# Kernel optimization log

Hardware: AMD Instinct MI355X
Metric: run time of the kernel (lower is better)

The kernel has to match this reference:

```python
import jax, jax.numpy as jnp
import numpy as np

E = 2048        # embed_dim
H = 16          # num_heads
D = 128         # head_dim
K = 4           # num_hyper_nodes (timelines)
N = 4096        # seq_len
B = 1           # batch (module asserts batch==1)
CAP_FACTOR = 1.25
CAP = int(N / K * CAP_FACTOR)   # 1280, static
ROPE_BASE = 10000.0
SCALE = D ** -0.5
NEG_INF = jnp.float32(-1e30)


def setup_inputs() -> dict:
    key = jax.random.key(0)
    ks = jax.random.split(key, 10)
    def xavier(k, shape):
        fan_in, fan_out = shape[0], shape[1]
        lim = np.sqrt(6.0 / (fan_in + fan_out))
        return jax.random.uniform(k, shape, jnp.float32, -lim, lim)
    return {
        'x':   jax.random.normal(ks[0], (B, N, E), jnp.float32),
        # weights stored (in, out); equivalent to torch Linear weight.T
        'Wq':  xavier(ks[1], (E, H * D)),
        'Wk':  xavier(ks[2], (E, H * D)),
        'Wv':  xavier(ks[3], (E, H * D)),
        'Wo':  xavier(ks[4], (H * D, E)),
        'Wr1': xavier(ks[5], (E, E // 2)),
        'br1': jnp.zeros((E // 2,), jnp.float32),
        'Wr2': xavier(ks[6], (E // 2, K)),
        'br2': jnp.zeros((K,), jnp.float32),
    }


def _rope_tables():
    # local positions: arange(CAP) (use_local_rope=True)
    inv_freq = 1.0 / (ROPE_BASE ** (jnp.arange(0, D, 2, dtype=jnp.float32) / D))
    freqs = jnp.arange(CAP, dtype=jnp.float32)[:, None] * inv_freq[None, :]  # (CAP, D/2)
    emb = jnp.concatenate([freqs, freqs], axis=-1)  # (CAP, D)
    return jnp.cos(emb), jnp.sin(emb)


def _rotate_half(t):
    return jnp.concatenate([-t[..., D // 2:], t[..., :D // 2]], axis=-1)


def reference(x, Wq, Wk, Wv, Wo, Wr1, br1, Wr2, br2):
    # --- expert-choice routing ---
    h = jax.nn.gelu(x @ Wr1 + br1, approximate=False)      # (B, N, E/2)
    scores = h @ Wr2 + br2                                  # (B, N, K)
    scores_t = scores[0].T                                  # (K, N)
    topk_scores, topk_idx = jax.lax.top_k(scores_t, CAP)    # (K, CAP)
    sel_w = jax.nn.softmax(topk_scores, axis=-1)            # (K, CAP)
    aux_loss = -jnp.mean(jnp.max(scores, axis=-1))

    # --- projections ---
    q = (x @ Wq).reshape(B, N, H, D).transpose(0, 2, 1, 3)  # (B, H, N, D)
    k = (x @ Wk).reshape(B, N, H, D).transpose(0, 2, 1, 3)
    v = (x @ Wv).reshape(B, N, H, D).transpose(0, 2, 1, 3)

    cos, sin = _rope_tables()                               # (CAP, D)
    causal = jnp.tril(jnp.ones((CAP, CAP), bool))

    def timeline(idx, w):
        # gather this timeline's tokens
        qt = q[:, :, idx]                                   # (B, H, CAP, D)
        kt = k[:, :, idx]
        vt = v[:, :, idx]
        qt = qt * cos + _rotate_half(qt) * sin
        kt = kt * cos + _rotate_half(kt) * sin
        att = jnp.einsum('bhqd,bhkd->bhqk', qt, kt) * SCALE
        att = jnp.where(causal, att, NEG_INF)
        att = jax.nn.softmax(att, axis=-1)
        o = jnp.einsum('bhqk,bhkd->bhqd', att, vt)          # (B, H, CAP, D)
        return o * w[None, None, :, None]                   # weighted combine

    outs = jax.vmap(timeline)(topk_idx, sel_w)              # (K, B, H, CAP, D)

    # scatter back: sum contributions over timelines
    idx_flat = topk_idx.reshape(-1)                         # (K*CAP,)
    vals = outs.transpose(1, 2, 0, 3, 4).reshape(B, H, K * CAP, D)
    out = jnp.zeros((B, H, N, D), x.dtype).at[:, :, idx_flat, :].add(vals)

    out = out.transpose(0, 2, 1, 3).reshape(B, N, H * D) @ Wo  # (B, N, E)
    return out, aux_loss
```

## Files before the change

kernel.cpp:

```cpp
#include <hip/hip_runtime.h>
#include <cstdint>
#include <cstddef>

#define N_TOK 4096
#define E_DIM 2048
#define NH    16
#define DH    128
#define KEXP  4
#define CAPN  1280
#define NTILE 20
#define QKV_STRIDE 6144
#define SCALE_QK 0.08838834764831845f
#define LOG2E    1.4426950408889634f
#define NEG_BIG -1e30f

typedef __attribute__((ext_vector_type(4))) float f32x4;
typedef __attribute__((ext_vector_type(8))) short s16x8;

__device__ __forceinline__ float bf2f(unsigned short u){
  union{unsigned int i; float fl;} c; c.i = ((unsigned int)u)<<16; return c.fl;
}
__device__ __forceinline__ unsigned short f2bf(float x){
  union{float fl; unsigned int i;} c; c.fl=x;
  return (unsigned short)((c.i + 0x7FFFu + ((c.i>>16)&1u))>>16);
}
__device__ __forceinline__ f32x4 mfma_bf16(s16x8 a, s16x8 b, f32x4 c){
  asm("v_mfma_f32_16x16x32_bf16 %0, %1, %2, %0" : "+v"(c) : "v"(a), "v"(b));
  return c;
}
__device__ __forceinline__ void gl_lds16(const unsigned short* g, unsigned short* l){
  __builtin_amdgcn_global_load_lds(
      (const __attribute__((address_space(1))) unsigned int*)g,
      (__attribute__((address_space(3))) unsigned int*)l, 16, 0, 0);
}

__global__ __launch_bounds__(256) void conv_x_kernel(const float* __restrict__ x,
    unsigned short* __restrict__ hi, unsigned short* __restrict__ lo, int n4){
  int idx = blockIdx.x*256 + threadIdx.x;
  if (idx >= n4) return;
  float4 v = ((const float4*)x)[idx];
  float ar[4] = {v.x, v.y, v.z, v.w};
  union{ unsigned short u[4]; uint2 q; } H, L;
  #pragma unroll
  for(int i=0;i<4;i++){
    unsigned short h = f2bf(ar[i]);
    H.u[i] = h;
    L.u[i] = f2bf(ar[i] - bf2f(h));
  }
  ((uint2*)hi)[idx] = H.q;
  ((uint2*)lo)[idx] = L.q;
}

__global__ __launch_bounds__(256) void tconv_kernel(const float* __restrict__ W,
    unsigned short* __restrict__ Thi, unsigned short* __restrict__ Tlo, int R, int C){
  __shared__ float t[32][33];
  int tx = threadIdx.x, ty = threadIdx.y;
  int c0 = blockIdx.x*32, r0 = blockIdx.y*32;
  #pragma unroll
  for(int i=0;i<4;i++){
    int r = r0 + ty + i*8;
    t[ty+i*8][tx] = W[(size_t)r*C + c0 + tx];
  }
  __syncthreads();
  #pragma unroll
  for(int i=0;i<4;i++){
    int c = c0 + ty + i*8;
    float v = t[tx][ty+i*8];
    size_t o = (size_t)c*R + r0 + tx;
    unsigned short h = f2bf(v);
    Thi[o] = h;
    if (Tlo) Tlo[o] = f2bf(v - bf2f(h));
  }
}

__global__ __launch_bounds__(256) void tconv4_kernel(const float* __restrict__ W0,
    const float* __restrict__ W1, const float* __restrict__ W2, const float* __restrict__ W3,
    unsigned short* __restrict__ out){
  __shared__ float t[32][33];
  int z = blockIdx.z;
  const float* W = (z==0)?W0 : (z==1)?W1 : (z==2)?W2 : W3;
  unsigned short* T = out + (size_t)z*E_DIM*E_DIM;
  int tx = threadIdx.x, ty = threadIdx.y;
  int c0 = blockIdx.x*32, r0 = blockIdx.y*32;
  #pragma unroll
  for(int i=0;i<4;i++){
    int r = r0 + ty + i*8;
    t[ty+i*8][tx] = W[(size_t)r*E_DIM + c0 + tx];
  }
  __syncthreads();
  #pragma unroll
  for(int i=0;i<4;i++){
    int c = c0 + ty + i*8;
    T[(size_t)c*E_DIM + r0 + tx] = f2bf(t[tx][ty+i*8]);
  }
}

template<int OUTBF>
__global__ __launch_bounds__(512, 1) void gemm_p(
    const unsigned short* __restrict__ A, const unsigned short* __restrict__ Bt,
    void* __restrict__ Cp, int N, int Kd){
  __shared__ __align__(16) unsigned short lds[2][24576];
  const int tid = threadIdx.x;
  const int w = tid>>6, lane = tid&63, g = lane>>4, r16 = lane&15;
  const int wm = w>>2, wn = w&3;
  const int mb = blockIdx.y, nb = blockIdx.x;
  const unsigned short* Ab = A  + (size_t)mb*128*Kd;
  const unsigned short* Bb = Bt + (size_t)nb*256*Kd;
  const int NT = Kd >> 6;

  f32x4 acc[4][4];
  #pragma unroll
  for(int i=0;i<4;i++)
    #pragma unroll
    for(int j=0;j<4;j++) acc[i][j] = f32x4{0.f,0.f,0.f,0.f};

  auto stageA = [&](int buf, int ks, int t){
    int row = tid>>2, ch = tid&3;
    int sc = ch ^ ((row>>1)&3);
    gl_lds16(Ab + (size_t)row*Kd + t*64 + ks*32 + sc*8, &lds[buf][ks*4096 + tid*8]);
  };
  auto stageB = [&](int buf, int ks, int t){
    #pragma unroll
    for(int i=0;i<2;i++){
      int n = i*512 + tid;
      int row = n>>2, ch = n&3;
      int sc = ch ^ ((row>>1)&3);
      gl_lds16(Bb + (size_t)row*Kd + t*64 + ks*32 + sc*8, &lds[buf][8192 + ks*8192 + n*8]);
    }
  };
  const int xoff = (g ^ ((r16>>1)&3)) << 3;

  stageA(0,0,0); stageB(0,0,0);
  stageA(0,1,0); stageB(0,1,0);
  stageA(1,0,1); stageB(1,0,1);
  asm volatile("s_waitcnt vmcnt(6)" ::: "memory");
  __builtin_amdgcn_s_barrier();

  int cur = 0;
  for(int t=0; t<NT; ++t){
    const int nxt = cur^1;
    s16x8 af[4], bfv[4];
    #pragma unroll
    for(int mf=0;mf<4;mf++)
      af[mf] = *(const s16x8*)&lds[cur][(wm*64 + mf*16 + r16)*32 + xoff];
    #pragma unroll
    for(int nf=0;nf<4;nf++)
      bfv[nf] = *(const s16x8*)&lds[cur][8192 + (wn*64 + nf*16 + r16)*32 + xoff];
    if (t+1 < NT){
      stageA(nxt,1,t+1); stageB(nxt,1,t+1);
      asm volatile("s_waitcnt vmcnt(6)" ::: "memory");
    } else {
      asm volatile("s_waitcnt vmcnt(0)" ::: "memory");
    }
    __builtin_amdgcn_s_barrier();
    __builtin_amdgcn_s_setprio(1);
    #pragma unroll
    for(int mf=0;mf<4;mf++)
      #pragma unroll
      for(int nf=0;nf<4;nf++)
        acc[mf][nf] = mfma_bf16(af[mf], bfv[nf], acc[mf][nf]);
    __builtin_amdgcn_s_setprio(0);
    __builtin_amdgcn_s_barrier();
    #pragma unroll
    for(int mf=0;mf<4;mf++)
      af[mf] = *(const s16x8*)&lds[cur][4096 + (wm*64 + mf*16 + r16)*32 + xoff];
    #pragma unroll
    for(int nf=0;nf<4;nf++)
      bfv[nf] = *(const s16x8*)&lds[cur][16384 + (wn*64 + nf*16 + r16)*32 + xoff];
    if (t+2 < NT){
      stageA(cur,0,t+2); stageB(cur,0,t+2);
      asm volatile("s_waitcnt vmcnt(6)" ::: "memory");
    } else if (t+1 < NT){
      asm volatile("s_waitcnt vmcnt(3)" ::: "memory");
    } else {
      asm volatile("s_waitcnt vmcnt(0)" ::: "memory");
    }
    __builtin_amdgcn_s_barrier();
    __builtin_amdgcn_s_setprio(1);
    #pragma unroll
    for(int mf=0;mf<4;mf++)
      #pragma unroll
      for(int nf=0;nf<4;nf++)
        acc[mf][nf] = mfma_bf16(af[mf], bfv[nf], acc[mf][nf]);
    __builtin_amdgcn_s_setprio(0);
    __builtin_amdgcn_s_barrier();
    cur ^= 1;
  }

  const int rowb = mb*128 + wm*64, colb = nb*256 + wn*64;
  #pragma unroll
  for(int mf=0;mf<4;mf++)
    #pragma unroll
    for(int nf=0;nf<4;nf++)
      #pragma unroll
      for(int r=0;r<4;r++){
        int rr = rowb + mf*16 + 4*g + r;
        int cc = colb + nf*16 + r16;
        size_t o = (size_t)rr*N + cc;
        if (OUTBF) ((unsigned short*)Cp)[o] = f2bf(acc[mf][nf][r]);
        else       ((float*)Cp)[o] = acc[mf][nf][r];
      }
}

__global__ __launch_bounds__(512, 1) void gemm_router_p(
    const unsigned short* __restrict__ Ahi, const unsigned short* __restrict__ Alo,
    const unsigned short* __restrict__ Bhi, const unsigned short* __restrict__ Blo,
    const float* __restrict__ br1, float* __restrict__ H){
  __shared__ __align__(16) unsigned short lds[2][32768];
  const int tid = threadIdx.x;
  const int w = tid>>6, lane = tid&63, g = lane>>4, r16 = lane&15;
  const int wm = w>>2, wn = w&3;
  const int mb = blockIdx.y, nb = blockIdx.x;
  const unsigned short* AbH = Ahi + (size_t)mb*128*E_DIM;
  const unsigned short* AbL = Alo + (size_t)mb*128*E_DIM;
  const unsigned short* BbH = Bhi + (size_t)nb*128*E_DIM;
  const unsigned short* BbL = Blo + (size_t)nb*128*E_DIM;
  const int NT = E_DIM >> 6;

  f32x4 acc[4][2];
  #pragma unroll
  for(int i=0;i<4;i++){ acc[i][0]=f32x4{0.f,0.f,0.f,0.f}; acc[i][1]=f32x4{0.f,0.f,0.f,0.f}; }

  auto stage = [&](int buf, int ks, int t){
    int row = tid>>2, ch = tid&3;
    int sc = ch ^ ((row>>1)&3);
    size_t go = (size_t)row*E_DIM + t*64 + ks*32 + sc*8;
    unsigned short* base = &lds[buf][ks*16384];
    gl_lds16(AbH + go, base +         tid*8);
    gl_lds16(AbL + go, base +  4096 + tid*8);
    gl_lds16(BbH + go, base +  8192 + tid*8);
    gl_lds16(BbL + go, base + 12288 + tid*8);
  };
  const int xoff = (g ^ ((r16>>1)&3)) << 3;

  stage(0,0,0); stage(0,1,0); stage(1,0,1);
  asm volatile("s_waitcnt vmcnt(8)" ::: "memory");
  __builtin_amdgcn_s_barrier();

  int cur = 0;
  for(int t=0; t<NT; ++t){
    const int nxt = cur^1;
    #pragma unroll
    for(int ph=0; ph<2; ph++){
      const unsigned short* base = &lds[cur][ph*16384];
      s16x8 ah[4], al[4], bh[2], bl[2];
      #pragma unroll
      for(int mf=0;mf<4;mf++){
        int ro = (wm*64 + mf*16 + r16)*32 + xoff;
        ah[mf] = *(const s16x8*)&base[ro];
        al[mf] = *(const s16x8*)&base[4096 + ro];
      }
      #pragma unroll
      for(int nf=0;nf<2;nf++){
        int ro = (wn*32 + nf*16 + r16)*32 + xoff;
        bh[nf] = *(const s16x8*)&base[8192 + ro];
        bl[nf] = *(const s16x8*)&base[12288 + ro];
      }
      if (ph==0){
        if (t+1 < NT){ stage(nxt,1,t+1); asm volatile("s_waitcnt vmcnt(8)" ::: "memory"); }
        else         {                   asm volatile("s_waitcnt vmcnt(0)" ::: "memory"); }
      } else {
        if (t+2 < NT){ stage(cur,0,t+2); asm volatile("s_waitcnt vmcnt(8)" ::: "memory"); }
        else if (t+1 < NT){              asm volatile("s_waitcnt vmcnt(4)" ::: "memory"); }
        else              {              asm volatile("s_waitcnt vmcnt(0)" ::: "memory"); }
      }
      __builtin_amdgcn_s_barrier();
      __builtin_amdgcn_s_setprio(1);
      #pragma unroll
      for(int mf=0;mf<4;mf++)
        #pragma unroll
        for(int nf=0;nf<2;nf++){
          acc[mf][nf] = mfma_bf16(ah[mf], bh[nf], acc[mf][nf]);
          acc[mf][nf] = mfma_bf16(ah[mf], bl[nf], acc[mf][nf]);
          acc[mf][nf] = mfma_bf16(al[mf], bh[nf], acc[mf][nf]);
        }
      __builtin_amdgcn_s_setprio(0);
      __builtin_amdgcn_s_barrier();
    }
    cur ^= 1;
  }

  const int rowb = mb*128 + wm*64, colb = nb*128 + wn*32;
  #pragma unroll
  for(int mf=0;mf<4;mf++)
    #pragma unroll
    for(int nf=0;nf<2;nf++)
      #pragma unroll
      for(int r=0;r<4;r++){
        int rr = rowb + mf*16 + 4*g + r;
        int cc = colb + nf*16 + r16;
        float v = acc[mf][nf][r] + br1[cc];
        H[(size_t)rr*1024 + cc] = 0.5f*v*(1.0f + erff(v*0.70710678118654752f));
      }
}

__global__ __launch_bounds__(256) void scores_kernel(const float* __restrict__ h,
    const float* __restrict__ Wr2, const float* __restrict__ br2,
    float* __restrict__ scores, float* __restrict__ tokmax){
  int tid = threadIdx.x;
  int n = blockIdx.x*4 + (tid>>6);
  int lane = tid & 63;
  const float* hr = h + (size_t)n*1024;
  float s0=0,s1=0,s2=0,s3=0;
  #pragma unroll
  for(int i=0;i<16;i++){
    int j = lane + i*64;
    float hv = hr[j];
    float4 wv = *(const float4*)(Wr2 + (size_t)j*4);
    s0 += hv*wv.x; s1 += hv*wv.y; s2 += hv*wv.z; s3 += hv*wv.w;
  }
  #pragma unroll
  for(int m=32;m>=1;m>>=1){
    s0 += __shfl_xor(s0,m); s1 += __shfl_xor(s1,m);
    s2 += __shfl_xor(s2,m); s3 += __shfl_xor(s3,m);
  }
  if (lane==0){
    s0+=br2[0]; s1+=br2[1]; s2+=br2[2]; s3+=br2[3];
    scores[n*4+0]=s0; scores[n*4+1]=s1; scores[n*4+2]=s2; scores[n*4+3]=s3;
    tokmax[n]=fmaxf(fmaxf(s0,s1),fmaxf(s2,s3));
  }
}

__global__ __launch_bounds__(1024) void aux_kernel(const float* __restrict__ tokmax, float* __restrict__ out_aux){
  __shared__ float red[1024];
  int t = threadIdx.x;
  red[t] = tokmax[t] + tokmax[t+1024] + tokmax[t+2048] + tokmax[t+3072];
  __syncthreads();
  for(int k=512;k>=1;k>>=1){ if(t<k) red[t]+=red[t+k]; __syncthreads(); }
  if (t==0) out_aux[0] = -red[0]/4096.0f;
}

__global__ __launch_bounds__(256) void rank_kernel(const float* __restrict__ scores,
    int* __restrict__ topk_idx, float* __restrict__ topv, int* __restrict__ rank_of){
  __shared__ unsigned long long keys[4096];
  const int e = blockIdx.y, blk = blockIdx.x, tid = threadIdx.x;
  for(int i=tid;i<4096;i+=256){
    unsigned u = __float_as_uint(scores[i*4+e]);
    unsigned m = (u & 0x80000000u) ? ~u : (u | 0x80000000u);
    keys[i] = (((unsigned long long)m)<<32) | (unsigned)(4095-i);
  }
  __syncthreads();
  const int i = blk*256 + tid;
  const unsigned long long mykey = keys[i];
  int cnt = 0;
  #pragma unroll 8
  for(int j=0;j<4096;j++) cnt += (keys[j] > mykey) ? 1 : 0;
  if (cnt < CAPN){
    topk_idx[e*CAPN + cnt] = i;
    topv[e*CAPN + cnt]     = scores[i*4+e];
    rank_of[e*4096 + i]    = cnt;
  } else {
    rank_of[e*4096 + i]    = -1;
  }
}

__global__ __launch_bounds__(1024) void selw_kernel(const float* __restrict__ topv,
    float* __restrict__ sel_w){
  __shared__ float red[1024];
  const int e = blockIdx.x, t = threadIdx.x;
  const float mx = topv[e*CAPN];
  float p0 = expf(topv[e*CAPN + t] - mx);
  float p1 = (t + 1024 < CAPN) ? expf(topv[e*CAPN + t + 1024] - mx) : 0.f;
  red[t] = p0 + p1;
  __syncthreads();
  for(int k=512;k>=1;k>>=1){ if(t<k) red[t]+=red[t+k]; __syncthreads(); }
  const float denom = red[0];
  sel_w[e*CAPN + t] = p0/denom;
  if (t + 1024 < CAPN) sel_w[e*CAPN + t + 1024] = p1/denom;
}

__global__ __launch_bounds__(256) void rope_kernel(float* __restrict__ cosT, float* __restrict__ sinT){
  int idx = blockIdx.x*256 + threadIdx.x;
  int p = idx>>6, dm = idx&63;
  float inv = powf(10000.0f, -(float)dm/64.0f);
  float ang = (float)p*inv;
  cosT[idx]=cosf(ang);
  sinT[idx]=sinf(ang);
}

__global__ __launch_bounds__(256) void prerope_k_kernel(const unsigned short* __restrict__ kb,
    const int* __restrict__ topk_idx, const float* __restrict__ cosT, const float* __restrict__ sinT,
    unsigned short* __restrict__ Kg){
  int idx = blockIdx.x*256 + threadIdx.x;
  int ch = idx & 15;
  int rest = idx >> 4;
  int rank = rest % CAPN;
  int he = rest / CAPN;
  int e = he >> 4, h = he & 15;
  int tok = topk_idx[e*CAPN + rank];
  int d0 = ch*8;
  const unsigned short* krow = kb + (size_t)tok*QKV_STRIDE + h*DH;
  unsigned short held[8], part[8];
  *(uint4*)held = *(const uint4*)(krow + d0);
  *(uint4*)part = *(const uint4*)(krow + (d0^64));
  const float* cr = cosT + rank*64;
  const float* sr = sinT + rank*64;
  float sgn = (d0<64) ? -1.f : 1.f;
  unsigned short outv[8];
  #pragma unroll
  for(int jj=0;jj<8;jj++){
    int dm = (d0+jj)&63;
    outv[jj] = f2bf(bf2f(held[jj])*cr[dm] + sgn*bf2f(part[jj])*sr[dm]);
  }
  int t = rank >> 6, row = rank & 63;
  size_t tbase = ((size_t)(he)*NTILE + t) * 8192;
  *(uint4*)(Kg + tbase + row*128 + ((ch ^ (row&7))<<3)) = *(uint4*)outv;
}

__global__ __launch_bounds__(256) void prev_kernel(const unsigned short* __restrict__ vb,
    const int* __restrict__ topk_idx, unsigned short* __restrict__ Vg){
  __shared__ __align__(16) unsigned short T2[128][72];
  int bid = blockIdx.x;
  int t = bid % NTILE, h = (bid/NTILE) & 15, e = bid/(NTILE*NH);
  int tid = threadIdx.x, lane = tid & 63, dchb = tid >> 6;
  int tok = topk_idx[e*CAPN + t*64 + lane];
  const unsigned short* vrow = vb + (size_t)tok*QKV_STRIDE + h*DH;
  #pragma unroll
  for(int i=0;i<4;i++){
    int d0 = (dchb + i*4)*8;
    unsigned short vv[8];
    *(uint4*)vv = *(const uint4*)(vrow + d0);
    #pragma unroll
    for(int j=0;j<8;j++) T2[d0+j][lane] = vv[j];
  }
  __syncthreads();
  unsigned short* out = Vg + ((size_t)(e*NH+h)*NTILE + t)*8192;
  #pragma unroll
  for(int i=0;i<4;i++){
    int c = i*256 + tid;
    int d = c>>3, ch = c&7;
    *(uint4*)(out + d*64 + ((ch ^ (d&7))<<3)) = *(const uint4*)&T2[d][ch*8];
  }
}

__global__ __launch_bounds__(256) void attn_kernel(
    const unsigned short* __restrict__ qb,
    const unsigned short* __restrict__ Kg, const unsigned short* __restrict__ Vg,
    const int* __restrict__ topk_idx, const float* __restrict__ sel_w,
    const float* __restrict__ cosT, const float* __restrict__ sinT,
    unsigned short* __restrict__ oexp){
  __shared__ __align__(16) unsigned short KsA[2][8192];
  __shared__ __align__(16) unsigned short Vs[8192];
  __shared__ __align__(16) unsigned short Ps[4][16][72];
  const int id = blockIdx.x;
  const int xcd = id & 7, s_ = id >> 3;
  const int qt = NTILE - 1 - (s_ % NTILE);
  const int grp = (s_ / NTILE)*8 + xcd;
  const int e = grp >> 4, hh = grp & 15;
  const int tid = threadIdx.x, w = tid>>6, lane = tid&63, g = lane>>4, r16 = lane&15;
  const int* idxE = topk_idx + e*CAPN;
  const unsigned short* Kgb = Kg + (size_t)(e*NH+hh)*CAPN*DH;
  const unsigned short* Vgb = Vg + (size_t)(e*NH+hh)*CAPN*DH;

  s16x8 aq[4];
  {
    int qr = qt*64 + w*16 + r16;
    int tok = idxE[qr];
    const unsigned short* qrow = qb + (size_t)tok*QKV_STRIDE + hh*DH;
    const float* cr = cosT + qr*64;
    const float* sr = sinT + qr*64;
    #pragma unroll
    for(int s=0;s<4;s++){
      int d0 = s*32 + 8*g;
      unsigned short held[8], part[8];
      *(uint4*)held = *(const uint4*)(qrow + d0);
      *(uint4*)part = *(const uint4*)(qrow + (d0^64));
      float sgn = (d0<64) ? -1.f : 1.f;
      union{ s16x8 v; unsigned short u[8]; } fr;
      #pragma unroll
      for(int jj=0;jj<8;jj++){
        int dm = (d0+jj)&63;
        float val = bf2f(held[jj])*cr[dm] + sgn*bf2f(part[jj])*sr[dm];
        fr.u[jj] = f2bf(val * (SCALE_QK*LOG2E));
      }
      aq[s] = fr.v;
    }
  }
  float m_r[4], l_r[4];
  f32x4 o[8];
  #pragma unroll
  for(int r=0;r<4;r++){ m_r[r]=-INFINITY; l_r[r]=0.f; }
  #pragma unroll
  for(int f2=0;f2<8;f2++) o[f2]=f32x4{0.f,0.f,0.f,0.f};

  #pragma unroll
  for(int i=0;i<4;i++){ int c=i*256+tid; gl_lds16(Kgb + c*8, &KsA[0][c*8]); }
  #pragma unroll
  for(int i=0;i<4;i++){ int c=i*256+tid; gl_lds16(Vgb + c*8, &Vs[c*8]); }
  asm volatile("s_waitcnt vmcnt(4)" ::: "memory");
  __builtin_amdgcn_s_barrier();

  for(int kt=0; kt<=qt; kt++){
    const int cur = kt & 1;
    if (kt < qt){
      const unsigned short* Ksrc = Kgb + (size_t)(kt+1)*8192;
      #pragma unroll
      for(int i=0;i<4;i++){ int c=i*256+tid; gl_lds16(Ksrc + c*8, &KsA[cur^1][c*8]); }
    }
    f32x4 sfr[4];
    #pragma unroll
    for(int fc=0;fc<4;fc++){
      f32x4 a4 = f32x4{0.f,0.f,0.f,0.f};
      const int row = fc*16 + r16;
      #pragma unroll
      for(int s=0;s<4;s++){
        s16x8 bk = *(const s16x8*)&KsA[cur][row*128 + (((s*4+g) ^ (r16&7))<<3)];
        a4 = mfma_bf16(aq[s], bk, a4);
      }
      sfr[fc] = a4;
    }
    if (kt==qt){
      #pragma unroll
      for(int fc=0;fc<4;fc++)
        #pragma unroll
        for(int r=0;r<4;r++){
          int qrank  = qt*64 + w*16 + 4*g + r;
          int kvrank = kt*64 + fc*16 + r16;
          if (kvrank > qrank) sfr[fc][r] = NEG_BIG;
        }
    }
    float corr[4];
    bool need = false;
    #pragma unroll
    for(int r=0;r<4;r++){
      float mx = fmaxf(fmaxf(sfr[0][r],sfr[1][r]), fmaxf(sfr[2][r],sfr[3][r]));
      #pragma unroll
      for(int mk=1;mk<16;mk<<=1) mx = fmaxf(mx, __shfl_xor(mx,mk));
      float nm = fmaxf(m_r[r], mx);
      need = need || (nm > m_r[r]);
      corr[r] = exp2f(m_r[r]-nm);
      m_r[r] = nm;
    }
    if (__any(need)){
      #pragma unroll
      for(int f2=0;f2<8;f2++)
        #pragma unroll
        for(int r=0;r<4;r++) o[f2][r] *= corr[r];
      #pragma unroll
      for(int r=0;r<4;r++) l_r[r] *= corr[r];
    }
    float rs[4] = {0.f,0.f,0.f,0.f};
    #pragma unroll
    for(int fc=0;fc<4;fc++)
      #pragma unroll
      for(int r=0;r<4;r++){
        float p = exp2f(sfr[fc][r] - m_r[r]);
        rs[r] += p;
        Ps[w][4*g+r][fc*16+r16] = f2bf(p);
      }
    #pragma unroll
    for(int r=0;r<4;r++){
      float ts = rs[r];
      #pragma unroll
      for(int mk=1;mk<16;mk<<=1) ts += __shfl_xor(ts,mk);
      l_r[r] += ts;
    }
    if (kt < qt) asm volatile("s_waitcnt vmcnt(4)" ::: "memory");
    else         asm volatile("s_waitcnt vmcnt(0)" ::: "memory");
    __builtin_amdgcn_s_barrier();
    #pragma unroll
    for(int ks=0;ks<2;ks++){
      s16x8 pa = *(const s16x8*)&Ps[w][r16][ks*32 + 8*g];
      #pragma unroll
      for(int fd=0;fd<8;fd++){
        const int row = fd*16 + r16;
        s16x8 vf = *(const s16x8*)&Vs[row*64 + (((ks*4+g) ^ (r16&7))<<3)];
        o[fd] = mfma_bf16(pa, vf, o[fd]);
      }
    }
    __builtin_amdgcn_s_barrier();
    if (kt < qt){
      const unsigned short* Vsrc = Vgb + (size_t)(kt+1)*8192;
      #pragma unroll
      for(int i=0;i<4;i++){ int c=i*256+tid; gl_lds16(Vsrc + c*8, &Vs[c*8]); }
      asm volatile("s_waitcnt vmcnt(4)" ::: "memory");
      __builtin_amdgcn_s_barrier();
    }
  }
  #pragma unroll
  for(int r=0;r<4;r++){
    int qrank = qt*64 + w*16 + 4*g + r;
    float fac = sel_w[e*CAPN + qrank] / l_r[r];
    #pragma unroll
    for(int fd=0;fd<8;fd++){
      oexp[((size_t)(e*CAPN + qrank))*E_DIM + hh*DH + fd*16 + r16] = f2bf(o[fd][r]*fac);
    }
  }
}

__global__ __launch_bounds__(256) void acc_kernel(const unsigned short* __restrict__ oexp,
    const int* __restrict__ rank_of, unsigned short* __restrict__ accb){
  int n = blockIdx.x, t = threadIdx.x;
  int base = t*8;
  float s[8] = {0,0,0,0,0,0,0,0};
  #pragma unroll
  for(int e=0;e<4;e++){
    int r = rank_of[e*4096+n];
    if (r>=0){
      union{uint4 q; unsigned short u[8];} ld;
      ld.q = *(const uint4*)(oexp + ((size_t)(e*CAPN+r))*E_DIM + base);
      #pragma unroll
      for(int j2=0;j2<8;j2++) s[j2] += bf2f(ld.u[j2]);
    }
  }
  union{uint4 q; unsigned short u[8];} st;
  #pragma unroll
  for(int j2=0;j2<8;j2++) st.u[j2] = f2bf(s[j2]);
  *(uint4*)(accb + (size_t)n*E_DIM + base) = st.q;
}

extern "C" void kernel_launch(void* const* d_in, const int* in_sizes, int n_in,
                              void* d_out, int out_size, void* d_ws, size_t ws_size,
                              hipStream_t stream) {
  const float* x   = (const float*)d_in[0];
  const float* Wq  = (const float*)d_in[1];
  const float* Wk  = (const float*)d_in[2];
  const float* Wv  = (const float*)d_in[3];
  const float* Wo  = (const float*)d_in[4];
  const float* Wr1 = (const float*)d_in[5];
  const float* br1 = (const float*)d_in[6];
  const float* Wr2 = (const float*)d_in[7];
  const float* br2 = (const float*)d_in[8];

  char* ws = (char*)d_ws;
  size_t off = 0;
  auto alloc = [&](size_t bytes)->void*{
    void* p = ws + off;
    off += (bytes + 255) & ~(size_t)255;
    return p;
  };
  unsigned short* xhi   = (unsigned short*)alloc((size_t)N_TOK*E_DIM*2);
  unsigned short* xlo   = (unsigned short*)alloc((size_t)N_TOK*E_DIM*2);
  unsigned short* wr1hi = (unsigned short*)alloc((size_t)E_DIM*1024*2);
  unsigned short* wr1lo = (unsigned short*)alloc((size_t)E_DIM*1024*2);
  unsigned short* wqkvT = (unsigned short*)alloc((size_t)3*E_DIM*E_DIM*2);
  unsigned short* woT   = (unsigned short*)alloc((size_t)E_DIM*E_DIM*2);
  void* hv = alloc((size_t)KEXP*NH*CAPN*DH*2);
  float* hbuf = (float*)hv;
  unsigned short* Vg = (unsigned short*)hv;
  float* scores = (float*)alloc((size_t)N_TOK*4*4);
  float* tokmax = (float*)alloc((size_t)N_TOK*4);
  int*   topkI  = (int*)alloc((size_t)KEXP*CAPN*4);
  float* topv   = (float*)alloc((size_t)KEXP*CAPN*4);
  float* selw   = (float*)alloc((size_t)KEXP*CAPN*4);
  int*   rankof = (int*)alloc((size_t)KEXP*N_TOK*4);
  float* cosT   = (float*)alloc((size_t)CAPN*64*4);
  float* sinT   = (float*)alloc((size_t)CAPN*64*4);
  unsigned short* qkvbuf = (unsigned short*)alloc((size_t)N_TOK*QKV_STRIDE*2);
  unsigned short* oexp = (unsigned short*)alloc((size_t)KEXP*CAPN*E_DIM*2);
  unsigned short* accb = (unsigned short*)alloc((size_t)N_TOK*E_DIM*2);
  if (off > ws_size) return;

  unsigned short* Kg = xlo;

  conv_x_kernel<<<(N_TOK*E_DIM/4+255)/256, 256, 0, stream>>>(x, xhi, xlo, N_TOK*E_DIM/4);
  tconv_kernel<<<dim3(1024/32, E_DIM/32), dim3(32,8), 0, stream>>>(Wr1, wr1hi, wr1lo, E_DIM, 1024);
  tconv4_kernel<<<dim3(E_DIM/32, E_DIM/32, 4), dim3(32,8), 0, stream>>>(Wq, Wk, Wv, Wo, wqkvT);

  gemm_router_p<<<dim3(8, 32), 512, 0, stream>>>(xhi, xlo, wr1hi, wr1lo, br1, hbuf);
  scores_kernel<<<N_TOK/4, 256, 0, stream>>>(hbuf, Wr2, br2, scores, tokmax);
  aux_kernel<<<1, 1024, 0, stream>>>(tokmax, ((float*)d_out) + (size_t)N_TOK*E_DIM);
  rank_kernel<<<dim3(16, KEXP), 256, 0, stream>>>(scores, topkI, topv, rankof);
  selw_kernel<<<KEXP, 1024, 0, stream>>>(topv, selw);
  rope_kernel<<<CAPN*64/256, 256, 0, stream>>>(cosT, sinT);

  gemm_p<1><<<dim3(QKV_STRIDE/256, N_TOK/128), 512, 0, stream>>>(xhi, wqkvT, qkvbuf, QKV_STRIDE, E_DIM);

  prerope_k_kernel<<<KEXP*NH*CAPN*16/256, 256, 0, stream>>>(qkvbuf + E_DIM, topkI, cosT, sinT, Kg);
  prev_kernel<<<KEXP*NH*NTILE, 256, 0, stream>>>(qkvbuf + 2*E_DIM, topkI, Vg);

  attn_kernel<<<KEXP*NH*NTILE, 256, 0, stream>>>(qkvbuf, Kg, Vg, topkI, selw, cosT, sinT, oexp);

  acc_kernel<<<N_TOK, 256, 0, stream>>>(oexp, rankof, accb);

  gemm_p<0><<<dim3(E_DIM/256, N_TOK/128), 512, 0, stream>>>(accb, woT, (float*)d_out, E_DIM, E_DIM);
}
```

Before: 448.3 us.

## Replace double-buffered GEMM K-loop with 5-slot ring, prefetch depth four

The projection GEMM's K loop moves from two 64-wide buffers, each split into two halves, to a five-slot ring of 32-wide K panels, with four panels kept in flight. Each iteration now uses one barrier instead of four and reads from a slot that was loaded several steps earlier. The goal is to hide global-to-LDS latency more deeply and cut synchronisation overhead. In exchange LDS use rises from 96KB to 120KB, and each iteration does less MFMA work between waits.

Result: no change. 445.9 us (-0.5%).

```diff
diff --git a/kernel.cpp b/kernel.cpp
--- a/kernel.cpp
+++ b/kernel.cpp
@@ -99,14 +99,14 @@
 __global__ __launch_bounds__(512, 1) void gemm_p(
     const unsigned short* __restrict__ A, const unsigned short* __restrict__ Bt,
     void* __restrict__ Cp, int N, int Kd){
-  __shared__ __align__(16) unsigned short lds[2][24576];
+  __shared__ __align__(16) unsigned short lds[5*12288];
   const int tid = threadIdx.x;
   const int w = tid>>6, lane = tid&63, g = lane>>4, r16 = lane&15;
   const int wm = w>>2, wn = w&3;
   const int mb = blockIdx.y, nb = blockIdx.x;
   const unsigned short* Ab = A  + (size_t)mb*128*Kd;
   const unsigned short* Bb = Bt + (size_t)nb*256*Kd;
-  const int NT = Kd >> 6;
+  const int PMAX = Kd >> 5;
 
   f32x4 acc[4][4];
   #pragma unroll
@@ -114,45 +114,39 @@
     #pragma unroll
     for(int j=0;j<4;j++) acc[i][j] = f32x4{0.f,0.f,0.f,0.f};
 
-  auto stageA = [&](int buf, int ks, int t){
-    int row = tid>>2, ch = tid&3;
-    int sc = ch ^ ((row>>1)&3);
-    gl_lds16(Ab + (size_t)row*Kd + t*64 + ks*32 + sc*8, &lds[buf][ks*4096 + tid*8]);
-  };
-  auto stageB = [&](int buf, int ks, int t){
+  auto stageP = [&](int Pst, int slot){
+    unsigned short* base = &lds[slot*12288];
+    const int col = Pst*32;
+    {
+      int row = tid>>2, ch = tid&3;
+      int sc = ch ^ ((row>>1)&3);
+      gl_lds16(Ab + (size_t)row*Kd + col + sc*8, base + tid*8);
+    }
     #pragma unroll
     for(int i=0;i<2;i++){
       int n = i*512 + tid;
-      int row = n>>2, ch = n&3;
-      int sc = ch ^ ((row>>1)&3);
-      gl_lds16(Bb + (size_t)row*Kd + t*64 + ks*32 + sc*8, &lds[buf][8192 + ks*8192 + n*8]);
+      int rw = n>>2, c2 = n&3;
+      int s2 = c2 ^ ((rw>>1)&3);
+      gl_lds16(Bb + (size_t)rw*Kd + col + s2*8, base + 4096 + n*8);
     }
   };
   const int xoff = (g ^ ((r16>>1)&3)) << 3;
 
-  stageA(0,0,0); stageB(0,0,0);
-  stageA(0,1,0); stageB(0,1,0);
-  stageA(1,0,1); stageB(1,0,1);
-  asm volatile("s_waitcnt vmcnt(6)" ::: "memory");
+  stageP(0,0); stageP(1,1); stageP(2,2); stageP(3,3);
+  asm volatile("s_waitcnt vmcnt(9)" ::: "memory");
   __builtin_amdgcn_s_barrier();
 
-  int cur = 0;
-  for(int t=0; t<NT; ++t){
-    const int nxt = cur^1;
+  int sR = 0, sW = 4;
+  for(int P=0; P<PMAX; ++P){
+    const unsigned short* base = &lds[sR*12288];
     s16x8 af[4], bfv[4];
     #pragma unroll
     for(int mf=0;mf<4;mf++)
-      af[mf] = *(const s16x8*)&lds[cur][(wm*64 + mf*16 + r16)*32 + xoff];
+      af[mf] = *(const s16x8*)&base[(wm*64 + mf*16 + r16)*32 + xoff];
     #pragma unroll
     for(int nf=0;nf<4;nf++)
-      bfv[nf] = *(const s16x8*)&lds[cur][8192 + (wn*64 + nf*16 + r16)*32 + xoff];
-    if (t+1 < NT){
-      stageA(nxt,1,t+1); stageB(nxt,1,t+1);
-      asm volatile("s_waitcnt vmcnt(6)" ::: "memory");
-    } else {
-      asm volatile("s_waitcnt vmcnt(0)" ::: "memory");
-    }
-    __builtin_amdgcn_s_barrier();
+      bfv[nf] = *(const s16x8*)&base[4096 + (wn*64 + nf*16 + r16)*32 + xoff];
+    if (P+4 < PMAX) stageP(P+4, sW);
     __builtin_amdgcn_s_setprio(1);
     #pragma unroll
     for(int mf=0;mf<4;mf++)
@@ -160,31 +154,13 @@
       for(int nf=0;nf<4;nf++)
         acc[mf][nf] = mfma_bf16(af[mf], bfv[nf], acc[mf][nf]);
     __builtin_amdgcn_s_setprio(0);
+    if      (P+4 < PMAX) asm volatile("s_waitcnt vmcnt(9)" ::: "memory");
+    else if (P+3 < PMAX) asm volatile("s_waitcnt vmcnt(6)" ::: "memory");
+    else if (P+2 < PMAX) asm volatile("s_waitcnt vmcnt(3)" ::: "memory");
+    else                 asm volatile("s_waitcnt vmcnt(0)" ::: "memory");
     __builtin_amdgcn_s_barrier();
-    #pragma unroll
-    for(int mf=0;mf<4;mf++)
-      af[mf] = *(const s16x8*)&lds[cur][4096 + (wm*64 + mf*16 + r16)*32 + xoff];
-    #pragma unroll
-    for(int nf=0;nf<4;nf++)
-      bfv[nf] = *(const s16x8*)&lds[cur][16384 + (wn*64 + nf*16 + r16)*32 + xoff];
-    if (t+2 < NT){
-      stageA(cur,0,t+2); stageB(cur,0,t+2);
-      asm volatile("s_waitcnt vmcnt(6)" ::: "memory");
-    } else if (t+1 < NT){
-      asm volatile("s_waitcnt vmcnt(3)" ::: "memory");
-    } else {
-      asm volatile("s_waitcnt vmcnt(0)" ::: "memory");
-    }
-    __builtin_amdgcn_s_barrier();
-    __builtin_amdgcn_s_setprio(1);
-    #pragma unroll
-    for(int mf=0;mf<4;mf++)
-      #pragma unroll
-      for(int nf=0;nf<4;nf++)
-        acc[mf][nf] = mfma_bf16(af[mf], bfv[nf], acc[mf][nf]);
-    __builtin_amdgcn_s_setprio(0);
-    __builtin_amdgcn_s_barrier();
-    cur ^= 1;
+    sR = (sR==4) ? 0 : sR+1;
+    sW = (sW==4) ? 0 : sW+1;
   }
 
   const int rowb = mb*128 + wm*64, colb = nb*256 + wn*64;
```
